# Kernel optimization log

Measured on AMD Instinct MI355X. Metric: run time of the kernel, lower is better.

The kernel has to match this reference:

```python
import jax, jax.numpy as jnp
import numpy as np
from jax import lax

# IVF+PQ search (FAISS IVF1024,PQ8x8 with nprobe=32, by_residual=False variant):
# 1) coarse quantizer: L2 distance of each query to nlist centroids, keep top nprobe lists
# 2) ADC: per-query LUT of squared distances between query subvectors and PQ codebooks,
#    database distance = sum over subquantizers of LUT gathered at the stored codes
# 3) mask database vectors whose IVF list was not probed, return indices of top_k smallest

NPROBE = 32  # top_n_centroids
BIG = jnp.float32(1e30)


def setup_inputs() -> dict:
    key = jax.random.key(0)
    ks = jax.random.split(key, 5)
    Q, D = 256, 128
    M, K = 8, 256          # pq_subvecs, 2**pq_nbits
    dsub = D // M          # 16
    nlist = 1024
    N = 250_000            # database size
    queries = jax.random.normal(ks[0], (Q, D), dtype=jnp.float32)
    centroids = jax.random.normal(ks[1], (nlist, D), dtype=jnp.float32)
    codebooks = jax.random.normal(ks[2], (M, K, dsub), dtype=jnp.float32)
    db_codes = jax.random.randint(ks[3], (N, M), 0, K, dtype=jnp.int32)
    db_list = jax.random.randint(ks[4], (N,), 0, nlist, dtype=jnp.int32)
    return {"queries": queries, "centroids": centroids, "codebooks": codebooks,
            "db_codes": db_codes, "db_list": db_list, "top_k": 100}


def _masked_adc_distances(queries, centroids, codebooks, db_codes, db_list):
    Q, D = queries.shape
    nlist = centroids.shape[0]
    M, K, dsub = codebooks.shape
    # ---- coarse quantizer: ||q - c||^2 over [Q, nlist] ----
    coarse = (jnp.sum(queries * queries, -1, keepdims=True)
              + jnp.sum(centroids * centroids, -1)[None, :]
              - 2.0 * queries @ centroids.T)
    _, probed = lax.top_k(-coarse, NPROBE)                      # [Q, NPROBE] list ids
    probe_mask = jnp.zeros((Q, nlist), dtype=bool).at[
        jnp.arange(Q)[:, None], probed].set(True)               # [Q, nlist]
    allowed = probe_mask[:, db_list]                            # [Q, N]
    # ---- PQ ADC lookup table: ||q_sub - codeword||^2, [Q, M, K] ----
    qs = queries.reshape(Q, M, dsub)
    lut = (jnp.sum(qs * qs, -1)[:, :, None]
           + jnp.sum(codebooks * codebooks, -1)[None, :, :]
           - 2.0 * jnp.einsum('qmd,mkd->qmk', qs, codebooks))   # [Q, M, K]
    # ---- accumulate gathered LUT entries over subquantizers ----
    dist = lut[:, 0, db_codes[:, 0]]                            # [Q, N]
    for m in range(1, M):
        dist = dist + lut[:, m, db_codes[:, m]]
    return jnp.where(allowed, dist, BIG)


def reference(queries, centroids, codebooks, db_codes, db_list, top_k):
    dist = _masked_adc_distances(queries, centroids, codebooks, db_codes, db_list)
    _, indices = lax.top_k(-dist, top_k)                        # smallest distances
    return indices
```

## Files before the change

### kernel.cpp

```cpp
#include <hip/hip_runtime.h>

#define DDIM 128
#define MSUB 8
#define KCODE 256
#define DSUB 16
#define NLIST 1024
#define NPROBE 32
#define TOPK 100
#define HBINS 4096
#define COLL_CAP 2048
#define RCAP 10
#define SCHUNK 1024
#define STHREADS 512


__device__ __forceinline__ float xla_sumsq128(const float* x) {
  float s[16];
  #pragma unroll
  for (int j = 0; j < 16; ++j) {
    float p0 = __fmul_rn(x[j],       x[j]);
    float p1 = __fmul_rn(x[j + 16],  x[j + 16]);
    float p2 = __fmul_rn(x[j + 32],  x[j + 32]);
    float p3 = __fmul_rn(x[j + 48],  x[j + 48]);
    float p4 = __fmul_rn(x[j + 64],  x[j + 64]);
    float p5 = __fmul_rn(x[j + 80],  x[j + 80]);
    float p6 = __fmul_rn(x[j + 96],  x[j + 96]);
    float p7 = __fmul_rn(x[j + 112], x[j + 112]);
    float r0 = __fadd_rn(p0, p4);
    float r1 = __fadd_rn(p1, p5);
    float r2 = __fadd_rn(p2, p6);
    float r3 = __fadd_rn(p3, p7);
    s[j] = __fadd_rn(__fadd_rn(r0, r1), __fadd_rn(r2, r3));
  }
  float a[8], b[4], c[2];
  #pragma unroll
  for (int j = 0; j < 8; ++j) a[j] = __fadd_rn(s[j], s[j + 8]);
  #pragma unroll
  for (int j = 0; j < 4; ++j) b[j] = __fadd_rn(a[j], a[j + 4]);
  #pragma unroll
  for (int j = 0; j < 2; ++j) c[j] = __fadd_rn(b[j], b[j + 2]);
  return __fadd_rn(c[0], c[1]);
}

__device__ __forceinline__ float xla_sumsq16(const float* x) {
  float p[16];
  #pragma unroll
  for (int j = 0; j < 16; ++j) p[j] = __fmul_rn(x[j], x[j]);
  float s8[8], s4[4], s2[2];
  #pragma unroll
  for (int j = 0; j < 8; ++j) s8[j] = __fadd_rn(p[j], p[j + 8]);
  #pragma unroll
  for (int j = 0; j < 4; ++j) s4[j] = __fadd_rn(s8[j], s8[j + 4]);
  #pragma unroll
  for (int j = 0; j < 2; ++j) s2[j] = __fadd_rn(s4[j], s4[j + 2]);
  return __fadd_rn(s2[0], s2[1]);
}

__device__ __forceinline__ float chain_dot16(const float* a, const float* b) {
  float dot = 0.f;
  #pragma unroll
  for (int d = 0; d < DSUB; ++d) dot = __fmaf_rn(a[d], b[d], dot);
  return dot;
}

__device__ __forceinline__ float adc_dist(const float* lut, unsigned long long code) {
  float d = lut[(unsigned)(code & 255ULL)];
  d = __fadd_rn(d, lut[256  + (unsigned)((code >> 8)  & 255ULL)]);
  d = __fadd_rn(d, lut[512  + (unsigned)((code >> 16) & 255ULL)]);
  d = __fadd_rn(d, lut[768  + (unsigned)((code >> 24) & 255ULL)]);
  d = __fadd_rn(d, lut[1024 + (unsigned)((code >> 32) & 255ULL)]);
  d = __fadd_rn(d, lut[1280 + (unsigned)((code >> 40) & 255ULL)]);
  d = __fadd_rn(d, lut[1536 + (unsigned)((code >> 48) & 255ULL)]);
  d = __fadd_rn(d, lut[1792 + (unsigned)((code >> 56) & 255ULL)]);
  return d;
}

__device__ __forceinline__ unsigned block_scan_incl(unsigned v, volatile unsigned* wsum,
                                                    int t, int nwaves) {
  int lane = t & 63, wid = t >> 6;
  #pragma unroll
  for (int off = 1; off < 64; off <<= 1) {
    unsigned u = __shfl_up(v, off, 64);
    if (lane >= off) v += u;
  }
  if (lane == 63) wsum[wid] = v;
  __syncthreads();
  if (wid == 0 && lane < nwaves) {
    unsigned wv = wsum[lane];
    #pragma unroll
    for (int off = 1; off < 16; off <<= 1) {
      unsigned u = __shfl_up(wv, off, 64);
      if (lane >= off) wv += u;
    }
    wsum[lane] = wv;
  }
  __syncthreads();
  return v + (wid > 0 ? wsum[wid - 1] : 0u);
}

__global__ __launch_bounds__(256) void k_front(const float* __restrict__ queries,
                                               const float* __restrict__ centroids,
                                               const int* __restrict__ db_list, int N,
                                               unsigned long long* __restrict__ keys_g,
                                               unsigned* __restrict__ counts) {
  const int t = threadIdx.x;
  const int r  = blockIdx.x % 5;
  const int b5 = blockIdx.x / 5;

  if (r == 0) {
    __shared__ unsigned hist_l[NLIST];
    for (int i = t; i < NLIST; i += 256) hist_l[i] = 0;
    __syncthreads();
    for (int n = b5 * 256 + t; n < N; n += 256 * 256)
      atomicAdd(&hist_l[db_list[n]], 1u);
    __syncthreads();
    for (int i = t; i < NLIST; i += 256)
      if (hist_l[i]) atomicAdd(&counts[i], hist_l[i]);
    return;
  }

  const int cid = b5 * 4 + (r - 1);
  const int qi = cid >> 2;
  const int part = cid & 3;
  __shared__ float qs[DDIM];
  if (t < DDIM) qs[t] = queries[qi * DDIM + t];
  __syncthreads();
  const float qq = xla_sumsq128(qs);
  const int c = part * 256 + t;
  const float* cr = centroids + (size_t)c * DDIM;
  float cbuf[DDIM];
  #pragma unroll
  for (int d = 0; d < DDIM; d += 4) {
    float4 cv = *(const float4*)(cr + d);
    cbuf[d] = cv.x; cbuf[d + 1] = cv.y; cbuf[d + 2] = cv.z; cbuf[d + 3] = cv.w;
  }
  const float cc = xla_sumsq128(cbuf);
  float dot = 0.f;
  #pragma unroll
  for (int d = 0; d < DDIM; ++d) dot = __fmaf_rn(qs[d], cbuf[d], dot);
  float dist = __fsub_rn(__fadd_rn(qq, cc), __fmul_rn(2.0f, dot));
  unsigned bits = __float_as_uint(dist);
  keys_g[(size_t)qi * NLIST + c] = ((unsigned long long)bits << 32) | (unsigned)c;
}

__global__ __launch_bounds__(STHREADS) void k_scatter(const int* __restrict__ db_list,
                                                      const int* __restrict__ db_codes, int N,
                                                      const unsigned* __restrict__ counts,
                                                      unsigned* __restrict__ cursor,
                                                      int4* __restrict__ pack) {
  __shared__ unsigned lhist[NLIST], lbase[NLIST], sbstart[NLIST];
  __shared__ unsigned wsum[16];
  const int t = threadIdx.x;
  const int base = blockIdx.x * SCHUNK;
  {
    unsigned c0 = counts[t * 2], c1 = counts[t * 2 + 1];
    unsigned sum2 = c0 + c1;
    unsigned incl = block_scan_incl(sum2, wsum, t, STHREADS / 64);
    unsigned excl = incl - sum2;
    sbstart[t * 2] = excl;
    sbstart[t * 2 + 1] = excl + c0;
  }
  for (int i = t; i < NLIST; i += STHREADS) lhist[i] = 0;
  __syncthreads();
  #pragma unroll
  for (int k = 0; k < SCHUNK / STHREADS; ++k) {
    int n = base + k * STHREADS + t;
    if (n < N) atomicAdd(&lhist[db_list[n]], 1u);
  }
  __syncthreads();
  for (int i = t; i < NLIST; i += STHREADS) {
    unsigned cnt = lhist[i];
    if (cnt) lbase[i] = sbstart[i] + atomicAdd(&cursor[i], cnt);
    lhist[i] = 0;
  }
  __syncthreads();
  #pragma unroll
  for (int k = 0; k < SCHUNK / STHREADS; ++k) {
    int n = base + k * STHREADS + t;
    if (n < N) {
      int l = db_list[n];
      unsigned pos = lbase[l] + atomicAdd(&lhist[l], 1u);
      const int4* cp = (const int4*)(db_codes + (size_t)n * MSUB);
      int4 c0 = cp[0], c1 = cp[1];
      unsigned lo = (unsigned)(c0.x & 255) | ((unsigned)(c0.y & 255) << 8) |
                    ((unsigned)(c0.z & 255) << 16) | ((unsigned)(c0.w & 255) << 24);
      unsigned hi = (unsigned)(c1.x & 255) | ((unsigned)(c1.y & 255) << 8) |
                    ((unsigned)(c1.z & 255) << 16) | ((unsigned)(c1.w & 255) << 24);
      pack[pos] = make_int4((int)lo, (int)hi, n, 0);
    }
  }
}

__global__ __launch_bounds__(1024, 1) void k_search(const float* __restrict__ queries,
                                                    const float* __restrict__ codebooks,
                                                    const unsigned long long* __restrict__ keys_g,
                                                    const unsigned* __restrict__ counts,
                                                    const int4* __restrict__ pack,
                                                    int* __restrict__ out) {
  const int qi = blockIdx.x;
  const int t = threadIdx.x;
  __shared__ float qs[DDIM];
  __shared__ float lut_s[MSUB * KCODE];
  __shared__ unsigned hist[HBINS];
  __shared__ unsigned long long coll[COLL_CAP];
  __shared__ unsigned bst[NLIST + 1];
  __shared__ unsigned pstart[NPROBE], pcum[NPROBE + 1];
  __shared__ unsigned wsum[16];
  __shared__ unsigned scnt;
  __shared__ int sT;

  if (t < DDIM) qs[t] = queries[qi * DDIM + t];
  const unsigned long long ckey = keys_g[(size_t)qi * NLIST + t];
  for (int i = t; i < HBINS; i += 1024) hist[i] = 0;
  if (t == 0) { scnt = 0; sT = HBINS - 1; }
  {
    unsigned v = counts[t];
    unsigned incl = block_scan_incl(v, wsum, t, 16);
    bst[t + 1] = incl;
    if (t == 0) bst[0] = 0;
  }
  __syncthreads();

  #pragma unroll
  for (int j = 0; j < (MSUB * KCODE) / 1024; ++j) {
    int idx = j * 1024 + t;
    const float* cb = codebooks + (size_t)idx * DSUB;
    const float* qsub = qs + (idx >> 8) * DSUB;
    float cbv[DSUB], qv[DSUB];
    #pragma unroll
    for (int d = 0; d < DSUB; d += 4) {
      float4 cv = *(const float4*)(cb + d);
      cbv[d] = cv.x; cbv[d + 1] = cv.y; cbv[d + 2] = cv.z; cbv[d + 3] = cv.w;
    }
    #pragma unroll
    for (int d = 0; d < DSUB; ++d) qv[d] = qsub[d];
    const float qq16 = xla_sumsq16(qv);
    const float cc16 = xla_sumsq16(cbv);
    const float dot16 = chain_dot16(qv, cbv);
    lut_s[idx] = __fsub_rn(__fadd_rn(qq16, cc16), __fmul_rn(2.0f, dot16));
  }

  atomicAdd(&hist[(unsigned)(ckey >> 51)], 1u);
  __syncthreads();
  {
    unsigned mysum = 0;
    #pragma unroll
    for (int i = 0; i < 4; ++i) mysum += hist[t * 4 + i];
    unsigned incl = block_scan_incl(mysum, wsum, t, 16);
    unsigned excl = incl - mysum;
    if (excl < NPROBE && NPROBE <= incl) {
      unsigned c2 = excl;
      #pragma unroll
      for (int i = 0; i < 4; ++i) {
        unsigned h = hist[t * 4 + i];
        if (c2 + h >= NPROBE) { sT = t * 4 + i; break; }
        c2 += h;
      }
    }
  }
  __syncthreads();
  {
    const int T32 = sT;
    if ((int)(ckey >> 51) <= T32) {
      unsigned p = atomicAdd(&scnt, 1u);
      if (p < 512) coll[p] = ckey;
    }
  }
  __syncthreads();
  {
    unsigned cnt = scnt; if (cnt > 512) cnt = 512;
    for (unsigned i = t; i < cnt; i += 1024) {
      unsigned long long k2 = coll[i];
      unsigned r = 0;
      for (unsigned j = 0; j < cnt; ++j) r += (coll[j] < k2) ? 1u : 0u;
      if (r < NPROBE) {
        unsigned l = (unsigned)(k2 & 0xffffffffULL);
        pstart[r] = bst[l];
        pcum[r + 1] = bst[l + 1] - bst[l];
      }
    }
  }
  __syncthreads();
  for (int i = t; i < HBINS; i += 1024) hist[i] = 0;
  if (t == 0) {
    scnt = 0; sT = HBINS - 1;
    unsigned acc = 0;
    pcum[0] = 0;
    for (int j = 1; j <= NPROBE; ++j) { acc += pcum[j]; pcum[j] = acc; }
  }
  __syncthreads();
  const unsigned total = pcum[NPROBE];

  unsigned long long regkey[RCAP];
  int lo = 0;
  #pragma unroll
  for (int s = 0; s < RCAP; ++s) {
    unsigned g = (unsigned)t + (unsigned)(s * 1024);
    if (g < total) {
      while (pcum[lo + 1] <= g) ++lo;
      unsigned addr = pstart[lo] + (g - pcum[lo]);
      int4 w = pack[addr];
      unsigned long long code = (unsigned)w.x | ((unsigned long long)(unsigned)w.y << 32);
      unsigned bits = __float_as_uint(adc_dist(lut_s, code));
      regkey[s] = ((unsigned long long)bits << 32) | (unsigned)w.z;
      atomicAdd(&hist[bits >> 19], 1u);
    }
  }
  for (unsigned g = (unsigned)t + RCAP * 1024; g < total; g += 1024) {
    while (pcum[lo + 1] <= g) ++lo;
    unsigned addr = pstart[lo] + (g - pcum[lo]);
    int4 w = pack[addr];
    unsigned long long code = (unsigned)w.x | ((unsigned long long)(unsigned)w.y << 32);
    unsigned bits = __float_as_uint(adc_dist(lut_s, code));
    atomicAdd(&hist[bits >> 19], 1u);
  }
  __syncthreads();

  {
    unsigned mysum = 0;
    #pragma unroll
    for (int i = 0; i < 4; ++i) mysum += hist[t * 4 + i];
    unsigned incl = block_scan_incl(mysum, wsum, t, 16);
    unsigned excl = incl - mysum;
    if (excl < TOPK && TOPK <= incl) {
      unsigned c = excl;
      #pragma unroll
      for (int i = 0; i < 4; ++i) {
        unsigned h = hist[t * 4 + i];
        if (c + h >= TOPK) { sT = t * 4 + i; break; }
        c += h;
      }
    }
  }
  __syncthreads();
  const int T = sT;

  {
    #pragma unroll
    for (int s = 0; s < RCAP; ++s) {
      unsigned g = (unsigned)t + (unsigned)(s * 1024);
      if (g < total) {
        unsigned long long k2 = regkey[s];
        if ((int)(unsigned)(k2 >> 51) <= T) {
          unsigned p = atomicAdd(&scnt, 1u);
          if (p < COLL_CAP) coll[p] = k2;
        }
      }
    }
    int lo2 = 0;
    for (unsigned g = (unsigned)t + RCAP * 1024; g < total; g += 1024) {
      while (pcum[lo2 + 1] <= g) ++lo2;
      unsigned addr = pstart[lo2] + (g - pcum[lo2]);
      int4 w = pack[addr];
      unsigned long long code = (unsigned)w.x | ((unsigned long long)(unsigned)w.y << 32);
      unsigned bits = __float_as_uint(adc_dist(lut_s, code));
      if ((int)(bits >> 19) <= T) {
        unsigned p = atomicAdd(&scnt, 1u);
        if (p < COLL_CAP) coll[p] = ((unsigned long long)bits << 32) | (unsigned)w.z;
      }
    }
  }
  __syncthreads();

  unsigned cnt = scnt;
  if (cnt > COLL_CAP) cnt = COLL_CAP;
  for (unsigned i = t; i < cnt; i += 1024) {
    unsigned long long key = coll[i];
    unsigned r = 0;
    for (unsigned j = 0; j < cnt; ++j) r += (coll[j] < key) ? 1u : 0u;
    if (r < TOPK) out[qi * TOPK + r] = (int)(key & 0xffffffffULL);
  }
}

extern "C" void kernel_launch(void* const* d_in, const int* in_sizes, int n_in,
                              void* d_out, int out_size, void* d_ws, size_t ws_size,
                              hipStream_t stream) {
  const float* queries   = (const float*)d_in[0];
  const float* centroids = (const float*)d_in[1];
  const float* codebooks = (const float*)d_in[2];
  const int*   db_codes  = (const int*)d_in[3];
  const int*   db_list   = (const int*)d_in[4];
  const int N = in_sizes[4];
  const int Q = in_sizes[0] / DDIM;
  int* out = (int*)d_out;

  char* p = (char*)d_ws;
  unsigned long long* keys_g = (unsigned long long*)p; p += (size_t)Q * NLIST * 8;
  unsigned* counts = (unsigned*)p;                  p += NLIST * 4;
  unsigned* cursor = (unsigned*)p;                  p += NLIST * 4;
  int4* pack = (int4*)p;                            p += (size_t)N * 16;

  hipMemsetAsync(counts, 0, (size_t)NLIST * 4 * 2, stream);

  k_front<<<Q * 4 + Q, 256, 0, stream>>>(queries, centroids, db_list, N, keys_g, counts);
  k_scatter<<<(N + SCHUNK - 1) / SCHUNK, STHREADS, 0, stream>>>(db_list, db_codes, N,
                                                                counts, cursor, pack);
  k_search<<<Q, 1024, 0, stream>>>(queries, codebooks, keys_g, counts, pack, out);
}
```

Measured before the change: 126.4 us.

## Move LUT build and probe selection into scatter kernel to overlap with scatter

Moves per-query LUT construction and coarse top-nprobe selection out of the 1024-thread search kernel into extra blocks of the scatter kernel, writing the LUT and probe ranges to global workspace. The search kernel then just loads the precomputed LUT and probe tables. This shortens the serial prologue of the one-block-per-CU search kernel and runs that work alongside the scatter. The cost is an extra global round trip for the LUT and probe data, plus more shared memory and block pressure in the combined prep kernel.

Result: no change. 124.1 us (-1.8%).

```diff
diff --git a/kernel.cpp b/kernel.cpp
--- a/kernel.cpp
+++ b/kernel.cpp
@@ -12,6 +12,7 @@
 #define RCAP 10
 #define SCHUNK 1024
 #define STHREADS 512
+#define PSTRIDE 66
 
 
 __device__ __forceinline__ float xla_sumsq128(const float* x) {
@@ -143,19 +144,130 @@
   keys_g[(size_t)qi * NLIST + c] = ((unsigned long long)bits << 32) | (unsigned)c;
 }
 
-__global__ __launch_bounds__(STHREADS) void k_scatter(const int* __restrict__ db_list,
-                                                      const int* __restrict__ db_codes, int N,
-                                                      const unsigned* __restrict__ counts,
-                                                      unsigned* __restrict__ cursor,
-                                                      int4* __restrict__ pack) {
+__global__ __launch_bounds__(STHREADS) void k_prep(const float* __restrict__ queries,
+                                                   const float* __restrict__ codebooks,
+                                                   const unsigned long long* __restrict__ keys_g,
+                                                   const int* __restrict__ db_list,
+                                                   const int* __restrict__ db_codes, int N,
+                                                   int Q,
+                                                   const unsigned* __restrict__ counts,
+                                                   unsigned* __restrict__ cursor,
+                                                   int4* __restrict__ pack,
+                                                   float* __restrict__ lut_g,
+                                                   unsigned* __restrict__ probe_g) {
+  const int t = threadIdx.x;
+  const int bid = blockIdx.x;
+
+  if (bid < Q) {
+    const int qi = bid;
+    __shared__ float qs[DDIM];
+    __shared__ unsigned hist[HBINS];
+    __shared__ unsigned long long coll[512];
+    __shared__ unsigned bst[NLIST + 1];
+    __shared__ unsigned pstart[NPROBE], pcum[NPROBE + 1];
+    __shared__ unsigned wsum[16];
+    __shared__ unsigned scnt;
+    __shared__ int sT;
+
+    if (t < DDIM) qs[t] = queries[qi * DDIM + t];
+    for (int i = t; i < HBINS; i += STHREADS) hist[i] = 0;
+    if (t == 0) { scnt = 0; sT = HBINS - 1; }
+    const unsigned long long k0 = keys_g[(size_t)qi * NLIST + t];
+    const unsigned long long k1 = keys_g[(size_t)qi * NLIST + t + STHREADS];
+    {
+      unsigned c0 = counts[2 * t], c1 = counts[2 * t + 1];
+      unsigned s2 = c0 + c1;
+      unsigned incl = block_scan_incl(s2, wsum, t, STHREADS / 64);
+      bst[2 * t + 1] = incl - c1;
+      bst[2 * t + 2] = incl;
+      if (t == 0) bst[0] = 0;
+    }
+    __syncthreads();
+
+    #pragma unroll
+    for (int j = 0; j < (MSUB * KCODE) / STHREADS; ++j) {
+      int idx = j * STHREADS + t;
+      const float* cb = codebooks + (size_t)idx * DSUB;
+      const float* qsub = qs + (idx >> 8) * DSUB;
+      float cbv[DSUB], qv[DSUB];
+      #pragma unroll
+      for (int d = 0; d < DSUB; d += 4) {
+        float4 cv = *(const float4*)(cb + d);
+        cbv[d] = cv.x; cbv[d + 1] = cv.y; cbv[d + 2] = cv.z; cbv[d + 3] = cv.w;
+      }
+      #pragma unroll
+      for (int d = 0; d < DSUB; ++d) qv[d] = qsub[d];
+      const float qq16 = xla_sumsq16(qv);
+      const float cc16 = xla_sumsq16(cbv);
+      const float dot16 = chain_dot16(qv, cbv);
+      lut_g[(size_t)qi * (MSUB * KCODE) + idx] =
+          __fsub_rn(__fadd_rn(qq16, cc16), __fmul_rn(2.0f, dot16));
+    }
+
+    atomicAdd(&hist[(unsigned)(k0 >> 51)], 1u);
+    atomicAdd(&hist[(unsigned)(k1 >> 51)], 1u);
+    __syncthreads();
+    {
+      unsigned mysum = 0;
+      #pragma unroll
+      for (int i = 0; i < HBINS / STHREADS; ++i) mysum += hist[t * (HBINS / STHREADS) + i];
+      unsigned incl = block_scan_incl(mysum, wsum, t, STHREADS / 64);
+      unsigned excl = incl - mysum;
+      if (excl < NPROBE && NPROBE <= incl) {
+        unsigned c2 = excl;
+        #pragma unroll
+        for (int i = 0; i < HBINS / STHREADS; ++i) {
+          unsigned h = hist[t * (HBINS / STHREADS) + i];
+          if (c2 + h >= NPROBE) { sT = t * (HBINS / STHREADS) + i; break; }
+          c2 += h;
+        }
+      }
+    }
+    __syncthreads();
+    {
+      const int T32 = sT;
+      if ((int)(k0 >> 51) <= T32) {
+        unsigned p = atomicAdd(&scnt, 1u);
+        if (p < 512) coll[p] = k0;
+      }
+      if ((int)(k1 >> 51) <= T32) {
+        unsigned p = atomicAdd(&scnt, 1u);
+        if (p < 512) coll[p] = k1;
+      }
+    }
+    __syncthreads();
+    {
+      unsigned cnt = scnt; if (cnt > 512) cnt = 512;
+      for (unsigned i = t; i < cnt; i += STHREADS) {
+        unsigned long long k2 = coll[i];
+        unsigned r = 0;
+        for (unsigned j = 0; j < cnt; ++j) r += (coll[j] < k2) ? 1u : 0u;
+        if (r < NPROBE) {
+          unsigned l = (unsigned)(k2 & 0xffffffffULL);
+          pstart[r] = bst[l];
+          pcum[r + 1] = bst[l + 1] - bst[l];
+        }
+      }
+    }
+    __syncthreads();
+    if (t == 0) {
+      unsigned acc = 0;
+      pcum[0] = 0;
+      for (int j = 1; j <= NPROBE; ++j) { acc += pcum[j]; pcum[j] = acc; }
+    }
+    __syncthreads();
+    if (t < NPROBE)     probe_g[qi * PSTRIDE + t] = pstart[t];
+    if (t < NPROBE + 1) probe_g[qi * PSTRIDE + NPROBE + t] = pcum[t];
+    return;
+  }
+
   __shared__ unsigned lhist[NLIST], lbase[NLIST], sbstart[NLIST];
-  __shared__ unsigned wsum[16];
-  const int t = threadIdx.x;
-  const int base = blockIdx.x * SCHUNK;
+  __shared__ unsigned wsum2[16];
+  const int base = (bid - Q) * SCHUNK;
   {
     unsigned c0 = counts[t * 2], c1 = counts[t * 2 + 1];
     unsigned sum2 = c0 + c1;
-    unsigned incl = block_scan_incl(sum2, wsum, t, STHREADS / 64);
+    unsigned incl = block_scan_incl(sum2, wsum2, t, STHREADS / 64);
     unsigned excl = incl - sum2;
     sbstart[t * 2] = excl;
     sbstart[t * 2 + 1] = excl + c0;
@@ -191,103 +303,26 @@
   }
 }
 
-__global__ __launch_bounds__(1024, 1) void k_search(const float* __restrict__ queries,
-                                                    const float* __restrict__ codebooks,
-                                                    const unsigned long long* __restrict__ keys_g,
-                                                    const unsigned* __restrict__ counts,
+__global__ __launch_bounds__(1024, 1) void k_search(const float* __restrict__ lut_g,
+                                                    const unsigned* __restrict__ probe_g,
                                                     const int4* __restrict__ pack,
                                                     int* __restrict__ out) {
   const int qi = blockIdx.x;
   const int t = threadIdx.x;
-  __shared__ float qs[DDIM];
   __shared__ float lut_s[MSUB * KCODE];
   __shared__ unsigned hist[HBINS];
   __shared__ unsigned long long coll[COLL_CAP];
-  __shared__ unsigned bst[NLIST + 1];
   __shared__ unsigned pstart[NPROBE], pcum[NPROBE + 1];
   __shared__ unsigned wsum[16];
   __shared__ unsigned scnt;
   __shared__ int sT;
 
-  if (t < DDIM) qs[t] = queries[qi * DDIM + t];
-  const unsigned long long ckey = keys_g[(size_t)qi * NLIST + t];
+  lut_s[t] = lut_g[(size_t)qi * (MSUB * KCODE) + t];
+  lut_s[1024 + t] = lut_g[(size_t)qi * (MSUB * KCODE) + 1024 + t];
   for (int i = t; i < HBINS; i += 1024) hist[i] = 0;
+  if (t < NPROBE)     pstart[t] = probe_g[qi * PSTRIDE + t];
+  if (t < NPROBE + 1) pcum[t] = probe_g[qi * PSTRIDE + NPROBE + t];
   if (t == 0) { scnt = 0; sT = HBINS - 1; }
-  {
-    unsigned v = counts[t];
-    unsigned incl = block_scan_incl(v, wsum, t, 16);
-    bst[t + 1] = incl;
-    if (t == 0) bst[0] = 0;
-  }
-  __syncthreads();
-
-  #pragma unroll
-  for (int j = 0; j < (MSUB * KCODE) / 1024; ++j) {
-    int idx = j * 1024 + t;
-    const float* cb = codebooks + (size_t)idx * DSUB;
-    const float* qsub = qs + (idx >> 8) * DSUB;
-    float cbv[DSUB], qv[DSUB];
-    #pragma unroll
-    for (int d = 0; d < DSUB; d += 4) {
-      float4 cv = *(const float4*)(cb + d);
-      cbv[d] = cv.x; cbv[d + 1] = cv.y; cbv[d + 2] = cv.z; cbv[d + 3] = cv.w;
-    }
-    #pragma unroll
-    for (int d = 0; d < DSUB; ++d) qv[d] = qsub[d];
-    const float qq16 = xla_sumsq16(qv);
-    const float cc16 = xla_sumsq16(cbv);
-    const float dot16 = chain_dot16(qv, cbv);
-    lut_s[idx] = __fsub_rn(__fadd_rn(qq16, cc16), __fmul_rn(2.0f, dot16));
-  }
-
-  atomicAdd(&hist[(unsigned)(ckey >> 51)], 1u);
-  __syncthreads();
-  {
-    unsigned mysum = 0;
-    #pragma unroll
-    for (int i = 0; i < 4; ++i) mysum += hist[t * 4 + i];
-    unsigned incl = block_scan_incl(mysum, wsum, t, 16);
-    unsigned excl = incl - mysum;
-    if (excl < NPROBE && NPROBE <= incl) {
-      unsigned c2 = excl;
-      #pragma unroll
-      for (int i = 0; i < 4; ++i) {
-        unsigned h = hist[t * 4 + i];
-        if (c2 + h >= NPROBE) { sT = t * 4 + i; break; }
-        c2 += h;
-      }
-    }
-  }
-  __syncthreads();
-  {
-    const int T32 = sT;
-    if ((int)(ckey >> 51) <= T32) {
-      unsigned p = atomicAdd(&scnt, 1u);
-      if (p < 512) coll[p] = ckey;
-    }
-  }
-  __syncthreads();
-  {
-    unsigned cnt = scnt; if (cnt > 512) cnt = 512;
-    for (unsigned i = t; i < cnt; i += 1024) {
-      unsigned long long k2 = coll[i];
-      unsigned r = 0;
-      for (unsigned j = 0; j < cnt; ++j) r += (coll[j] < k2) ? 1u : 0u;
-      if (r < NPROBE) {
-        unsigned l = (unsigned)(k2 & 0xffffffffULL);
-        pstart[r] = bst[l];
-        pcum[r + 1] = bst[l + 1] - bst[l];
-      }
-    }
-  }
-  __syncthreads();
-  for (int i = t; i < HBINS; i += 1024) hist[i] = 0;
-  if (t == 0) {
-    scnt = 0; sT = HBINS - 1;
-    unsigned acc = 0;
-    pcum[0] = 0;
-    for (int j = 1; j <= NPROBE; ++j) { acc += pcum[j]; pcum[j] = acc; }
-  }
   __syncthreads();
   const unsigned total = pcum[NPROBE];
 
@@ -389,11 +424,16 @@
   unsigned* counts = (unsigned*)p;                  p += NLIST * 4;
   unsigned* cursor = (unsigned*)p;                  p += NLIST * 4;
   int4* pack = (int4*)p;                            p += (size_t)N * 16;
+  float* lut_g = (float*)p;                         p += (size_t)Q * MSUB * KCODE * 4;
+  unsigned* probe_g = (unsigned*)p;                 p += (size_t)Q * PSTRIDE * 4;
+
+  const int nscat = (N + SCHUNK - 1) / SCHUNK;
 
   hipMemsetAsync(counts, 0, (size_t)NLIST * 4 * 2, stream);
 
   k_front<<<Q * 4 + Q, 256, 0, stream>>>(queries, centroids, db_list, N, keys_g, counts);
-  k_scatter<<<(N + SCHUNK - 1) / SCHUNK, STHREADS, 0, stream>>>(db_list, db_codes, N,
-                                                                counts, cursor, pack);
-  k_search<<<Q, 1024, 0, stream>>>(queries, codebooks, keys_g, counts, pack, out);
-}
+  k_prep<<<Q + nscat, STHREADS, 0, stream>>>(queries, codebooks, keys_g, db_list,
+                                             db_codes, N, Q, counts, cursor, pack,
+                                             lut_g, probe_g);
+  k_search<<<Q, 1024, 0, stream>>>(lut_g, probe_g, pack, out);
+}
```
